# Kernel optimization log

Measured on AMD Instinct MI355X. Metric: run time of the kernel, lower is better.

## Reference

```python
import jax, jax.numpy as jnp
import numpy as np

WINDOW_LENGTH = 8  # hop size used by overlap_and_add (matches init_kwargs)


def overlap_and_add(x, step):
    """x: [B, C, T, L] frames; returns [B, C, (T-1)*step + L].
    Requires L % step == 0 (standard Conv-TasNet overlap_and_add)."""
    B, C, T, L = x.shape
    k = L // step  # subframes per frame
    sub = x.reshape(B, C, T * k, step)
    # subframe j of frame t lands at output subframe t + j
    seg = (jnp.arange(T)[:, None] + jnp.arange(k)[None, :]).reshape(-1)
    out = jnp.zeros((B, C, T + k - 1, step), x.dtype).at[:, :, seg].add(sub)
    return out.reshape(B, C, (T + k - 1) * step)


def setup_inputs() -> dict:
    key = jax.random.key(0)
    k1, k2 = jax.random.split(key)
    B, C, D, T = 8, 2, 16, 128000
    x = jax.random.normal(k1, (B, C, D, T), dtype=jnp.float32)
    x_wave = jax.random.normal(k2, (B, D, T), dtype=jnp.float32)
    return {"x": x, "x_wave": x_wave, "pad_left": 8, "pad_right": 8}


def reference(x, x_wave, pad_left, pad_right):
    # x: [B, C, D, T] masks; x_wave: [B, D, T] encoder output
    x = x * x_wave[:, None]              # broadcast over speaker axis C
    x = jnp.transpose(x, (0, 1, 3, 2))   # [B, C, T, D] -> frames of length D
    y = overlap_and_add(x, WINDOW_LENGTH)  # [B, C, (T-1)*hop + D]
    if pad_right:
        y = y[:, :, pad_left:y.shape[-1] - pad_right]
    else:
        y = y[:, :, pad_left:]
    return y
```

## Files before the change

### kernel.cpp

```cpp
#include <hip/hip_runtime.h>


constexpr int B = 8;
constexpr int C = 2;
constexpr int D = 16;
constexpr int T = 128000;

__global__ __launch_bounds__(256) void oaa_seg_kernel(
    const float* __restrict__ x,
    const float* __restrict__ xw,
    float* __restrict__ out,
    int S)
{
    const int tid = blockIdx.x * 256 + threadIdx.x;
    const int seg = tid + 1;
    if (seg >= T) return;
    const int b = blockIdx.y;

    const float* xwb = xw + (size_t)b * (D * T);
    const float* xb  = x  + (size_t)b * (C * D * T);

    const int t0 = seg;
    const int t1 = seg - 1;

    float acc0[8], acc1[8];
#pragma unroll
    for (int d = 0; d < 8; ++d) {
        const float w0 = xwb[d * T + t0];
        const float w1 = xwb[(d + 8) * T + t1];
        acc0[d] = xb[d * T + t0] * w0
                + xb[(d + 8) * T + t1] * w1;
        acc1[d] = xb[(D + d) * T + t0] * w0
                + xb[(D + d + 8) * T + t1] * w1;
    }

    const size_t ob = (size_t)b * C * S;
    const int s0 = seg * 8 - 8;
    float4* o0 = (float4*)(out + ob + s0);
    float4* o1 = (float4*)(out + ob + S + s0);
    o0[0] = make_float4(acc0[0], acc0[1], acc0[2], acc0[3]);
    o0[1] = make_float4(acc0[4], acc0[5], acc0[6], acc0[7]);
    o1[0] = make_float4(acc1[0], acc1[1], acc1[2], acc1[3]);
    o1[1] = make_float4(acc1[4], acc1[5], acc1[6], acc1[7]);
}

extern "C" void kernel_launch(void* const* d_in, const int* in_sizes, int n_in,
                              void* d_out, int out_size, void* d_ws, size_t ws_size,
                              hipStream_t stream) {
    const float* x  = (const float*)d_in[0];
    const float* xw = (const float*)d_in[1];
    float* out = (float*)d_out;

    const int S = out_size / (B * C);
    const int nthreads = T - 1;
    const int nblk = (nthreads + 255) / 256;
    dim3 grid(nblk, B);
    oaa_seg_kernel<<<grid, dim3(256), 0, stream>>>(x, xw, out, S);
}
```

Before: 252.1 us.

## Stage input tiles in LDS with float4 loads before computing segments

Each block now cooperatively loads a 256-column tile (plus an 8-column halo) of all 48 input rows into shared memory with vectorized float4 global loads, then each thread reads its shifted taps from LDS. This replaces per-thread scalar global loads, each row read at two offsets, with one wide coalesced pass. It adds about 51 KB of shared memory per block and a barrier, which lowers occupancy. It also re-reads the 8-column halo from global memory in every block.

```diff
diff --git a/kernel.cpp b/kernel.cpp
--- a/kernel.cpp
+++ b/kernel.cpp
@@ -6,42 +6,64 @@
 constexpr int D = 16;
 constexpr int T = 128000;
 
-__global__ __launch_bounds__(256) void oaa_seg_kernel(
+constexpr int TILE    = 256;
+constexpr int NROW    = 48;
+constexpr int NC4     = 66;
+constexpr int LSTRIDE = 268;
+
+__global__ __launch_bounds__(256) void oaa_tile_kernel(
     const float* __restrict__ x,
     const float* __restrict__ xw,
     float* __restrict__ out,
     int S)
 {
-    const int tid = blockIdx.x * 256 + threadIdx.x;
-    const int seg = tid + 1;
-    if (seg >= T) return;
-    const int b = blockIdx.y;
+    __shared__ float lds[NROW * LSTRIDE];
 
-    const float* xwb = xw + (size_t)b * (D * T);
-    const float* xb  = x  + (size_t)b * (C * D * T);
+    const int b     = blockIdx.y;
+    const int tbase = blockIdx.x * TILE;
 
-    const int t0 = seg;
-    const int t1 = seg - 1;
+    const float* wb = xw + (size_t)b * (D * T);
+    const float* xb = x  + (size_t)b * (C * D * T);
 
-    float acc0[8], acc1[8];
+    for (int idx = threadIdx.x; idx < NROW * NC4; idx += 256) {
+        const int row  = idx / NC4;
+        const int col4 = idx - row * NC4;
+        const int gc   = tbase - 8 + col4 * 4;
+        const float* src = (row < 16) ? (wb + row * T) : (xb + (row - 16) * T);
+        float4 v = make_float4(0.f, 0.f, 0.f, 0.f);
+        if (gc >= 0) v = *(const float4*)(src + gc);
+        *(float4*)(&lds[row * LSTRIDE + col4 * 4]) = v;
+    }
+    __syncthreads();
+
+    const int j   = threadIdx.x;
+    const int seg = tbase + j;
+    if (seg >= 1 && seg < T) {
+        const int c0 = j + 8;
+        const int c1 = j + 7;
+
+        float acc0[8], acc1[8];
 #pragma unroll
-    for (int d = 0; d < 8; ++d) {
-        const float w0 = xwb[d * T + t0];
-        const float w1 = xwb[(d + 8) * T + t1];
-        acc0[d] = xb[d * T + t0] * w0
-                + xb[(d + 8) * T + t1] * w1;
-        acc1[d] = xb[(D + d) * T + t0] * w0
-                + xb[(D + d + 8) * T + t1] * w1;
+        for (int i = 0; i < 8; ++i) {
+            const float w0 = lds[i * LSTRIDE + c0];
+            const float w1 = lds[(i + 8) * LSTRIDE + c1];
+            const float a0 = lds[(16 + i) * LSTRIDE + c0];
+            const float a1 = lds[(24 + i) * LSTRIDE + c1];
+            const float b0 = lds[(32 + i) * LSTRIDE + c0];
+            const float b1 = lds[(40 + i) * LSTRIDE + c1];
+            acc0[i] = a0 * w0 + a1 * w1;
+            acc1[i] = b0 * w0 + b1 * w1;
+        }
+
+        const size_t ob = (size_t)b * C * S;
+        const int s0 = seg * 8 - 8;
+        float4* o0 = (float4*)(out + ob + s0);
+        float4* o1 = (float4*)(out + ob + S + s0);
+        o0[0] = make_float4(acc0[0], acc0[1], acc0[2], acc0[3]);
+        o0[1] = make_float4(acc0[4], acc0[5], acc0[6], acc0[7]);
+        o1[0] = make_float4(acc1[0], acc1[1], acc1[2], acc1[3]);
+        o1[1] = make_float4(acc1[4], acc1[5], acc1[6], acc1[7]);
     }
-
-    const size_t ob = (size_t)b * C * S;
-    const int s0 = seg * 8 - 8;
-    float4* o0 = (float4*)(out + ob + s0);
-    float4* o1 = (float4*)(out + ob + S + s0);
-    o0[0] = make_float4(acc0[0], acc0[1], acc0[2], acc0[3]);
-    o0[1] = make_float4(acc0[4], acc0[5], acc0[6], acc0[7]);
-    o1[0] = make_float4(acc1[0], acc1[1], acc1[2], acc1[3]);
-    o1[1] = make_float4(acc1[4], acc1[5], acc1[6], acc1[7]);
 }
 
 extern "C" void kernel_launch(void* const* d_in, const int* in_sizes, int n_in,
@@ -52,8 +74,7 @@
     float* out = (float*)d_out;
 
     const int S = out_size / (B * C);
-    const int nthreads = T - 1;
-    const int nblk = (nthreads + 255) / 256;
-    dim3 grid(nblk, B);
-    oaa_seg_kernel<<<grid, dim3(256), 0, stream>>>(x, xw, out, S);
+    const int ntile = T / TILE;
+    dim3 grid(ntile, B);
+    oaa_tile_kernel<<<grid, dim3(256), 0, stream>>>(x, xw, out, S);
 }
```

Measured after the change: 259.2 us. 2.8% more time.
